# Kernel optimization log

Measured on AMD Instinct MI355X. Metric: run time of the kernel, lower is better.

## Reference

```python
import jax, jax.numpy as jnp
import numpy as np

LAMBDA_D = 250.0
POS_MARGIN = 1.0
NEG_MARGIN = 0.2
BLOCK = 8          # block_size in the original
DIST_THRESH = 7.5  # correspondence threshold in pixels
EPS = 1e-12        # F.normalize eps


def _l2_normalize(x, axis):
    # matches torch.nn.functional.normalize: x / max(||x||_2, eps)
    n = jnp.linalg.norm(x, axis=axis, keepdims=True)
    return x / jnp.maximum(n, EPS)


def setup_inputs() -> dict:
    key = jax.random.key(0)
    k1, k2, k3 = jax.random.split(key, 3)
    b, d, hc, wc = 2, 256, 60, 80  # 480x640 image, block 8
    desc = jax.random.normal(k1, (b, d, hc, wc), dtype=jnp.float32)
    wrap_desc = jax.random.normal(k2, (b, d, hc, wc), dtype=jnp.float32)
    # realistic near-identity homographies (random H would warp everything off-image)
    H = jnp.eye(3, dtype=jnp.float32)[None] + 0.02 * jax.random.normal(k3, (b, 3, 3), dtype=jnp.float32)
    return {"desc": desc, "wrap_desc": wrap_desc, "H": H}


def reference(desc, wrap_desc, H):
    b, d, hc, wc = desc.shape
    n = hc * wc

    # cell-center coordinates in (row, col) order, shape (hc, wc, 2)
    coords = jnp.stack(
        jnp.meshgrid(jnp.arange(hc), jnp.arange(wc), indexing="ij"), axis=-1
    ).astype(jnp.float32) * BLOCK + BLOCK // 2

    # homogeneous (x, y, 1) points, shape (n, 3)
    xy1 = jnp.concatenate(
        [coords[..., 1:2], coords[..., 0:1], jnp.ones((hc, wc, 1), jnp.float32)],
        axis=-1,
    ).reshape(n, 3)

    # warp by homography: (b, n, 3)
    w = jnp.einsum("bij,nj->bni", H, xy1)
    wxy = w[..., :2] / w[..., 2:3]                       # (b, n, 2) in (x, y)
    warp = jnp.stack([wxy[..., 1], wxy[..., 0]], axis=-1).reshape(b, hc, wc, 2)  # (row, col)

    # distance between warped query centers and all cell centers: (b, hc, wc, hc, wc)
    dist = jnp.linalg.norm(coords[None, None, None] - warp[:, :, :, None, None, :], axis=-1)
    S = (dist <= DIST_THRESH).astype(desc.dtype)

    # unit-normalized descriptors, channel-last
    dn = _l2_normalize(jnp.transpose(desc, (0, 2, 3, 1)), axis=-1)       # (b, hc, wc, d)
    wn = _l2_normalize(jnp.transpose(wrap_desc, (0, 2, 3, 1)), axis=-1)  # (b, hc, wc, d)

    # full correlation volume via batched GEMM (same math as broadcast-sum)
    dot = jax.nn.relu(jnp.einsum("bijd,bkld->bijkl", dn, wn))           # (b,hc,wc,hc,wc)

    # normalize over warped-cell axis (k, l), then over query-cell axis (i, j)
    dot = _l2_normalize(dot.reshape(b, hc, wc, n), axis=3).reshape(b, hc, wc, hc, wc)
    dot = _l2_normalize(dot.reshape(b, n, hc, wc), axis=1).reshape(b, hc, wc, hc, wc)

    loss = LAMBDA_D * S * jax.nn.relu(POS_MARGIN - dot) + (1.0 - S) * jax.nn.relu(dot - NEG_MARGIN)
    # sum over (i,j,k,l) per image / n^2, then sum over batch == total sum / n^2
    return jnp.sum(loss) / float(n * n)
```

## Files before the change

### kernel.cpp

```cpp
#include <hip/hip_runtime.h>

#define HC 60
#define WCC 80
#define NCELL 4800
#define NP 4864
#define NB 38
#define DCH 256
#define BATCH 2
#define QT 64

typedef _Float16 half8 __attribute__((ext_vector_type(8)));
typedef float f32x4 __attribute__((ext_vector_type(4)));

__device__ __forceinline__ void gload_lds16(const void* gp, void* lp) {
  __builtin_amdgcn_global_load_lds(
      (const __attribute__((address_space(1))) void*)gp,
      (__attribute__((address_space(3))) void*)lp, 16, 0, 0);
}

__global__ __launch_bounds__(256) void warp_kernel(const float* __restrict__ H,
                                                   float* __restrict__ wout) {
  int idx = blockIdx.x * 256 + threadIdx.x;
  if (idx >= BATCH * NP) return;
  int b = idx / NP;
  int q = idx - b * NP;
  float wr = 1e9f, wc = 1e9f;
  if (q < NCELL) {
    int i = q / WCC;
    int j = q - i * WCC;
    float x = (float)(j * 8 + 4);
    float y = (float)(i * 8 + 4);
    const float* h = H + b * 9;
    float w0 = h[0] * x + h[1] * y + h[2];
    float w1 = h[3] * x + h[4] * y + h[5];
    float w2 = h[6] * x + h[7] * y + h[8];
    wr = w1 / w2;
    wc = w0 / w2;
  }
  wout[2 * idx]     = wr;
  wout[2 * idx + 1] = wc;
}

__global__ __launch_bounds__(256) void normalize_kernel(
    const float* __restrict__ desc, const float* __restrict__ wdesc,
    _Float16* __restrict__ dnp, _Float16* __restrict__ wnp) {
  __shared__ _Float16 vt[DCH][QT + 2];
  __shared__ float pss[4][QT];
  __shared__ float invq[QT];
  const int q0 = blockIdx.x * QT;
  const int which = blockIdx.y;
  const int b = blockIdx.z;
  const float* in = which ? wdesc : desc;
  _Float16* out = which ? wnp : dnp;
  const int tx = threadIdx.x & 63;
  const int ty = threadIdx.x >> 6;
  const int q = q0 + tx;
  float ss = 0.f;
  for (int cc = 0; cc < DCH / 4; ++cc) {
    const int c = cc * 4 + ty;
    float v = (q < NCELL) ? in[((size_t)b * DCH + c) * NCELL + q] : 0.f;
    vt[c][tx] = (_Float16)v;
    ss += v * v;
  }
  pss[ty][tx] = ss;
  __syncthreads();
  if (ty == 0) {
    float tot = pss[0][tx] + pss[1][tx] + pss[2][tx] + pss[3][tx];
    invq[tx] = 1.f / fmaxf(sqrtf(tot), 1e-12f);
  }
  __syncthreads();
  for (int it = 0; it < QT; ++it) {
    out[((size_t)b * NP + q0 + it) * DCH + threadIdx.x] =
        (_Float16)((float)vt[threadIdx.x][it] * invq[it]);
  }
}

union GemmSmem {
  struct { _Float16 As[128][64]; _Float16 Bs[128][64]; } g;
  _Float16 rp[128][132];
};

template <int MODE, bool STOREU>
__global__ __launch_bounds__(256) void gemm_kernel(
    const _Float16* __restrict__ A, const _Float16* __restrict__ Bm,
    const float* __restrict__ invr, const float* __restrict__ colscale,
    const float* __restrict__ warp, float* __restrict__ sqacc,
    float* __restrict__ lossp, _Float16* __restrict__ uout) {
  __shared__ GemmSmem sm;
  const int tid = threadIdx.x;
  const int wave = tid >> 6;
  const int lane = tid & 63;
  const int batch = blockIdx.z;
  const int row0 = blockIdx.y * 128;
  const int col0 = blockIdx.x * 128;
  const _Float16* Ab = A + ((size_t)batch * NP + row0) * DCH;
  const _Float16* Bb = Bm + ((size_t)batch * NP + col0) * DCH;

  const int wq_r = wave >> 1;
  const int wq_c = wave & 1;
  const int g = lane >> 4;
  const int cL = lane & 15;

  f32x4 acc[4][4] = {};

  const int srow = lane >> 3;
  const int scol = lane & 7;
  const int sc_swz = (scol ^ srow) * 8;

  for (int ks = 0; ks < 4; ++ks) {
#pragma unroll
    for (int c = 0; c < 4; ++c) {
      const int chunk = wave * 4 + c;
      const int r = chunk * 8 + srow;
      gload_lds16(Ab + (size_t)r * DCH + ks * 64 + sc_swz,
                  (char*)(&sm.g.As[0][0]) + chunk * 1024);
      gload_lds16(Bb + (size_t)r * DCH + ks * 64 + sc_swz,
                  (char*)(&sm.g.Bs[0][0]) + chunk * 1024);
    }
    __syncthreads();
#pragma unroll
    for (int kk = 0; kk < 2; ++kk) {
      half8 af[4], bf[4];
#pragma unroll
      for (int m = 0; m < 4; ++m) {
        const int row = wq_r * 64 + m * 16 + cL;
        const int c16 = (kk * 4 + g) ^ (row & 7);
        af[m] = *reinterpret_cast<const half8*>(
            (const char*)(&sm.g.As[0][0]) + row * 128 + c16 * 16);
      }
#pragma unroll
      for (int n = 0; n < 4; ++n) {
        const int row = wq_c * 64 + n * 16 + cL;
        const int c16 = (kk * 4 + g) ^ (row & 7);
        bf[n] = *reinterpret_cast<const half8*>(
            (const char*)(&sm.g.Bs[0][0]) + row * 128 + c16 * 16);
      }
#pragma unroll
      for (int m = 0; m < 4; ++m)
#pragma unroll
        for (int n = 0; n < 4; ++n)
          acc[m][n] =
              __builtin_amdgcn_mfma_f32_16x16x32_f16(af[m], bf[n], acc[m][n], 0, 0, 0);
    }
    __syncthreads();
  }

  if (MODE == 0 || MODE == 1) {
    float cs[4];
    if (MODE == 1) {
#pragma unroll
      for (int n = 0; n < 4; ++n)
        cs[n] = colscale[(size_t)batch * NP + col0 + wq_c * 64 + n * 16 + cL];
    }
    float rs[4][4];
#pragma unroll
    for (int m = 0; m < 4; ++m)
#pragma unroll
      for (int j = 0; j < 4; ++j) rs[m][j] = 0.f;
#pragma unroll
    for (int m = 0; m < 4; ++m)
#pragma unroll
      for (int n = 0; n < 4; ++n)
#pragma unroll
        for (int j = 0; j < 4; ++j) {
          float u = fmaxf(acc[m][n][j], 0.f);
          if (MODE == 1) u *= cs[n];
          rs[m][j] += u * u;
        }
#pragma unroll
    for (int m = 0; m < 4; ++m)
#pragma unroll
      for (int j = 0; j < 4; ++j) {
        float v = rs[m][j];
        v += __shfl_xor(v, 1, 64);
        v += __shfl_xor(v, 2, 64);
        v += __shfl_xor(v, 4, 64);
        v += __shfl_xor(v, 8, 64);
        if (cL == 0)
          atomicAdd(&sqacc[(size_t)batch * NP + row0 + wq_r * 64 + m * 16 + g * 4 + j], v);
      }
    if (STOREU) {
#pragma unroll
      for (int m = 0; m < 4; ++m)
#pragma unroll
        for (int n = 0; n < 4; ++n)
#pragma unroll
          for (int j = 0; j < 4; ++j)
            sm.rp[wq_r * 64 + m * 16 + g * 4 + j][wq_c * 64 + n * 16 + cL] =
                (_Float16)fmaxf(acc[m][n][j], 0.f);
      __syncthreads();
      const int rl = tid >> 4;
      const int uu = tid & 15;
#pragma unroll
      for (int p = 0; p < 8; ++p) {
        const int row = p * 16 + rl;
        half8 hv = *reinterpret_cast<const half8*>(&sm.rp[row][uu * 8]);
        *reinterpret_cast<half8*>(
            &uout[((size_t)batch * NP + row0 + row) * NP + col0 + uu * 8]) = hv;
      }
    }
  } else if (MODE == 2) {
    float cy[4], cx[4], ic[4];
    int cvalid[4];
#pragma unroll
    for (int n = 0; n < 4; ++n) {
      int ct = col0 + wq_c * 64 + n * 16 + cL;
      cvalid[n] = (ct < NCELL);
      int tk = ct / WCC;
      int tl = ct - tk * WCC;
      cy[n] = (float)(tk * 8 + 4);
      cx[n] = (float)(tl * 8 + 4);
      ic[n] = colscale[(size_t)batch * NP + ct];
    }
    float lsum = 0.f;
#pragma unroll
    for (int m = 0; m < 4; ++m)
#pragma unroll
      for (int j = 0; j < 4; ++j) {
        const int rq = row0 + wq_r * 64 + m * 16 + g * 4 + j;
        if (rq < NCELL) {
          const float ir = invr[(size_t)batch * NP + rq];
          const float wr = warp[((size_t)batch * NP + rq) * 2];
          const float wcol = warp[((size_t)batch * NP + rq) * 2 + 1];
#pragma unroll
          for (int n = 0; n < 4; ++n) {
            if (cvalid[n]) {
              float u = fmaxf(acc[m][n][j], 0.f);
              float v = u * ir * ic[n];
              float dr = cy[n] - wr;
              float dc = cx[n] - wcol;
              float pos = 250.f * fmaxf(1.f - v, 0.f);
              float neg = fmaxf(v - 0.2f, 0.f);
              lsum += (dr * dr + dc * dc <= 56.25f) ? pos : neg;
            }
          }
        }
      }
#pragma unroll
    for (int s = 1; s < 64; s <<= 1) lsum += __shfl_xor(lsum, s, 64);
    if (lane == 0) {
      int slot = (((batch * NB + blockIdx.y) * NB + blockIdx.x) << 2) | wave;
      lossp[slot] = lsum;
    }
  }
}

__global__ __launch_bounds__(256) void passB_kernel(const _Float16* __restrict__ u,
                                                    const float* __restrict__ r2,
                                                    float* __restrict__ c2) {
  const int b = blockIdx.z;
  const int lt = threadIdx.x & 63;
  const int lq = threadIdx.x >> 6;
  const int t0 = blockIdx.x * 512 + lt * 8;
  const int q0 = blockIdx.y * 64 + lq * 16;
  float s[8];
#pragma unroll
  for (int i = 0; i < 8; ++i) s[i] = 0.f;
  if (t0 < NP) {
    const _Float16* up = u + ((size_t)b * NP + q0) * NP + t0;
    const float* r2p = r2 + b * NP + q0;
#pragma unroll 4
    for (int q = 0; q < 16; ++q) {
      const float ir = 1.f / fmaxf(sqrtf(r2p[q]), 1e-12f);
      half8 h = *reinterpret_cast<const half8*>(up + (size_t)q * NP);
#pragma unroll
      for (int i = 0; i < 8; ++i) {
        float v = (float)h[i] * ir;
        s[i] += v * v;
      }
    }
  }
  __shared__ float red[4][64][9];
#pragma unroll
  for (int i = 0; i < 8; ++i) red[lq][lt][i] = s[i];
  __syncthreads();
  if (lq == 0 && t0 < NP) {
#pragma unroll
    for (int i = 0; i < 8; ++i) {
      float tot = red[0][lt][i] + red[1][lt][i] + red[2][lt][i] + red[3][lt][i];
      atomicAdd(&c2[b * NP + t0 + i], tot);
    }
  }
}

__global__ __launch_bounds__(256) void passC_kernel(const _Float16* __restrict__ u,
                                                    const float* __restrict__ r2,
                                                    const float* __restrict__ c2,
                                                    const float* __restrict__ warp,
                                                    float* __restrict__ lossp) {
  const int b = blockIdx.z;
  const int lt = threadIdx.x & 63;
  const int lq = threadIdx.x >> 6;
  const int t0 = blockIdx.x * 512 + lt * 8;
  const int q0 = blockIdx.y * 128 + lq * 32;
  float cy[8], cx[8], ic[8];
  bool val[8];
  const bool act = (t0 < NP);
#pragma unroll
  for (int i = 0; i < 8; ++i) {
    const int t = act ? (t0 + i) : 0;
    val[i] = act && (t < NCELL);
    const int tk = t / WCC;
    const int tl = t - tk * WCC;
    cy[i] = (float)(tk * 8 + 4);
    cx[i] = (float)(tl * 8 + 4);
    ic[i] = val[i] ? 1.f / fmaxf(sqrtf(c2[b * NP + t]), 1e-12f) : 0.f;
  }
  float lsum = 0.f;
  if (act) {
    const _Float16* up = u + ((size_t)b * NP + q0) * NP + t0;
#pragma unroll 4
    for (int q = 0; q < 32; ++q) {
      const int qq = q0 + q;
      const float ir = 1.f / fmaxf(sqrtf(r2[b * NP + qq]), 1e-12f);
      const float wr = warp[(size_t)(b * NP + qq) * 2];
      const float wc = warp[(size_t)(b * NP + qq) * 2 + 1];
      half8 h = *reinterpret_cast<const half8*>(up + (size_t)q * NP);
#pragma unroll
      for (int i = 0; i < 8; ++i) {
        if (val[i]) {
          float v = (float)h[i] * ir * ic[i];
          float dr = cy[i] - wr;
          float dc = cx[i] - wc;
          float pos = 250.f * fmaxf(1.f - v, 0.f);
          float neg = fmaxf(v - 0.2f, 0.f);
          lsum += (dr * dr + dc * dc <= 56.25f) ? pos : neg;
        }
      }
    }
  }
#pragma unroll
  for (int s = 1; s < 64; s <<= 1) lsum += __shfl_xor(lsum, s, 64);
  if (lt == 0)
    lossp[(((b * NB + blockIdx.y) * 10 + blockIdx.x) << 2) | lq] = lsum;
}

__global__ void finalize_inv(const float* __restrict__ sq, float* __restrict__ inv,
                             int count) {
  int i = blockIdx.x * 256 + threadIdx.x;
  if (i < count) inv[i] = 1.f / fmaxf(sqrtf(sq[i]), 1e-12f);
}

__global__ __launch_bounds__(1024) void loss_reduce(const float* __restrict__ lossp,
                                                    float* __restrict__ out, int count) {
  double s = 0.0;
  for (int i = threadIdx.x; i < count; i += 1024) s += (double)lossp[i];
#pragma unroll
  for (int k = 1; k < 64; k <<= 1) s += __shfl_xor(s, k, 64);
  __shared__ double sd[16];
  if ((threadIdx.x & 63) == 0) sd[threadIdx.x >> 6] = s;
  __syncthreads();
  if (threadIdx.x == 0) {
    double t = 0.0;
    for (int w = 0; w < 16; ++w) t += sd[w];
    out[0] = (float)(t / ((double)NCELL * (double)NCELL));
  }
}

extern "C" void kernel_launch(void* const* d_in, const int* in_sizes, int n_in,
                              void* d_out, int out_size, void* d_ws, size_t ws_size,
                              hipStream_t stream) {
  const float* desc  = (const float*)d_in[0];
  const float* wdesc = (const float*)d_in[1];
  const float* H     = (const float*)d_in[2];
  char* ws = (char*)d_ws;

  constexpr size_t SZ_HALF = (size_t)BATCH * NP * DCH * sizeof(_Float16);
  constexpr size_t SZ_WARP = (size_t)BATCH * NP * 2 * sizeof(float);
  constexpr size_t SZ_VEC  = (size_t)BATCH * NP * sizeof(float);
  constexpr size_t SZ_LOSS = (size_t)BATCH * NB * 10 * 4 * sizeof(float);
  constexpr size_t SZ_U    = (size_t)BATCH * NP * NP * sizeof(_Float16);
  constexpr size_t OFF_DNP  = 0;
  constexpr size_t OFF_WNP  = OFF_DNP + SZ_HALF;
  constexpr size_t OFF_WARP = OFF_WNP + SZ_HALF;
  constexpr size_t OFF_R2   = OFF_WARP + SZ_WARP;
  constexpr size_t OFF_C2   = OFF_R2 + SZ_VEC;
  constexpr size_t OFF_INVR = OFF_C2 + SZ_VEC;
  constexpr size_t OFF_INVC = OFF_INVR + SZ_VEC;
  constexpr size_t OFF_LOSS = OFF_INVC + SZ_VEC;
  constexpr size_t SZ_LOSS2 = (size_t)BATCH * NB * NB * 4 * sizeof(float);
  constexpr size_t OFF_U    = OFF_LOSS + (SZ_LOSS > SZ_LOSS2 ? SZ_LOSS : SZ_LOSS2);
  constexpr size_t TOTAL    = OFF_U + SZ_U;

  _Float16* dnp = (_Float16*)(ws + OFF_DNP);
  _Float16* wnp = (_Float16*)(ws + OFF_WNP);
  float* warp = (float*)(ws + OFF_WARP);
  float* r2   = (float*)(ws + OFF_R2);
  float* c2   = (float*)(ws + OFF_C2);
  float* invr = (float*)(ws + OFF_INVR);
  float* invc = (float*)(ws + OFF_INVC);
  float* lossp = (float*)(ws + OFF_LOSS);
  _Float16* u = (_Float16*)(ws + OFF_U);

  hipMemsetAsync(r2, 0, 2 * SZ_VEC, stream);

  warp_kernel<<<dim3((BATCH * NP + 255) / 256), 256, 0, stream>>>(H, warp);
  normalize_kernel<<<dim3(NP / QT, 2, BATCH), 256, 0, stream>>>(desc, wdesc, dnp, wnp);

  dim3 gg(NB, NB, BATCH);
  if (ws_size >= TOTAL) {
    gemm_kernel<0, true><<<gg, 256, 0, stream>>>(dnp, wnp, nullptr, nullptr, nullptr,
                                                 r2, nullptr, u);
    passB_kernel<<<dim3(10, 76, BATCH), 256, 0, stream>>>(u, r2, c2);
    passC_kernel<<<dim3(10, NB, BATCH), 256, 0, stream>>>(u, r2, c2, warp, lossp);
    loss_reduce<<<1, 1024, 0, stream>>>(lossp, (float*)d_out, BATCH * NB * 10 * 4);
  } else {
    gemm_kernel<0, false><<<gg, 256, 0, stream>>>(dnp, wnp, nullptr, nullptr, nullptr,
                                                  r2, nullptr, nullptr);
    finalize_inv<<<(BATCH * NP + 255) / 256, 256, 0, stream>>>(r2, invr, BATCH * NP);
    gemm_kernel<1, false><<<gg, 256, 0, stream>>>(wnp, dnp, nullptr, invr, nullptr,
                                                  c2, nullptr, nullptr);
    finalize_inv<<<(BATCH * NP + 255) / 256, 256, 0, stream>>>(c2, invc, BATCH * NP);
    gemm_kernel<2, false><<<gg, 256, 0, stream>>>(dnp, wnp, invr, invc, warp,
                                                  nullptr, lossp, nullptr);
    loss_reduce<<<1, 1024, 0, stream>>>(lossp, (float*)d_out, BATCH * NB * NB * 4);
  }
}
```

Baseline: 241.3 us.

## Split normalize into sumsq and transpose kernels, retile passB/passC, inline warp

```diff
diff --git a/kernel.cpp b/kernel.cpp
--- a/kernel.cpp
+++ b/kernel.cpp
@@ -7,10 +7,10 @@
 #define NB 38
 #define DCH 256
 #define BATCH 2
-#define QT 64
 
 typedef _Float16 half8 __attribute__((ext_vector_type(8)));
 typedef float f32x4 __attribute__((ext_vector_type(4)));
+typedef float float4v __attribute__((ext_vector_type(4)));
 
 __device__ __forceinline__ void gload_lds16(const void* gp, void* lp) {
   __builtin_amdgcn_global_load_lds(
@@ -41,37 +41,69 @@
   wout[2 * idx + 1] = wc;
 }
 
-__global__ __launch_bounds__(256) void normalize_kernel(
+__global__ __launch_bounds__(256) void sumsq_kernel(const float* __restrict__ desc,
+                                                    const float* __restrict__ wdesc,
+                                                    float* __restrict__ ss) {
+  const int b = blockIdx.z;
+  const int tensor = blockIdx.y >> 2;
+  const int c0 = (blockIdx.y & 3) * 64;
+  const int q = blockIdx.x * 256 + threadIdx.x;
+  const float* in = tensor ? wdesc : desc;
+  float s = 0.f;
+  if (q < NCELL) {
+    const float* p = in + ((size_t)b * DCH + c0) * NCELL + q;
+#pragma unroll 16
+    for (int c = 0; c < 64; ++c) {
+      float v = p[(size_t)c * NCELL];
+      s += v * v;
+    }
+  }
+  atomicAdd(&ss[((size_t)tensor * BATCH + b) * NP + q], s);
+}
+
+__global__ __launch_bounds__(256) void transpose_kernel(
     const float* __restrict__ desc, const float* __restrict__ wdesc,
-    _Float16* __restrict__ dnp, _Float16* __restrict__ wnp) {
-  __shared__ _Float16 vt[DCH][QT + 2];
-  __shared__ float pss[4][QT];
-  __shared__ float invq[QT];
-  const int q0 = blockIdx.x * QT;
-  const int which = blockIdx.y;
+    const float* __restrict__ ss, _Float16* __restrict__ dnp,
+    _Float16* __restrict__ wnp) {
+  __shared__ _Float16 vt[256][66];
+  __shared__ float iss[256];
   const int b = blockIdx.z;
-  const float* in = which ? wdesc : desc;
-  _Float16* out = which ? wnp : dnp;
-  const int tx = threadIdx.x & 63;
-  const int ty = threadIdx.x >> 6;
-  const int q = q0 + tx;
-  float ss = 0.f;
-  for (int cc = 0; cc < DCH / 4; ++cc) {
-    const int c = cc * 4 + ty;
-    float v = (q < NCELL) ? in[((size_t)b * DCH + c) * NCELL + q] : 0.f;
-    vt[c][tx] = (_Float16)v;
-    ss += v * v;
-  }
-  pss[ty][tx] = ss;
+  const int tensor = blockIdx.y >> 2;
+  const int c0 = (blockIdx.y & 3) * 64;
+  const int q0 = blockIdx.x * 256;
+  const float* in = tensor ? wdesc : desc;
+  _Float16* out = tensor ? wnp : dnp;
+  const int wave = threadIdx.x >> 6;
+  const int lane = threadIdx.x & 63;
+  {
+    float v = ss[((size_t)tensor * BATCH + b) * NP + q0 + threadIdx.x];
+    iss[threadIdx.x] = 1.f / fmaxf(sqrtf(v), 1e-12f);
+  }
+#pragma unroll
+  for (int i = 0; i < 16; ++i) {
+    const int c = c0 + wave * 16 + i;
+    const int q = q0 + lane * 4;
+    float4v v = {0.f, 0.f, 0.f, 0.f};
+    if (q + 3 < NCELL) {
+      v = *reinterpret_cast<const float4v*>(in + ((size_t)b * DCH + c) * NCELL + q);
+    } else {
+#pragma unroll
+      for (int k = 0; k < 4; ++k)
+        if (q + k < NCELL) v[k] = in[((size_t)b * DCH + c) * NCELL + q + k];
+    }
+#pragma unroll
+    for (int k = 0; k < 4; ++k) vt[lane * 4 + k][wave * 16 + i] = (_Float16)v[k];
+  }
   __syncthreads();
-  if (ty == 0) {
-    float tot = pss[0][tx] + pss[1][tx] + pss[2][tx] + pss[3][tx];
-    invq[tx] = 1.f / fmaxf(sqrtf(tot), 1e-12f);
-  }
-  __syncthreads();
-  for (int it = 0; it < QT; ++it) {
-    out[((size_t)b * NP + q0 + it) * DCH + threadIdx.x] =
-        (_Float16)((float)vt[threadIdx.x][it] * invq[it]);
+#pragma unroll
+  for (int p = 0; p < 8; ++p) {
+    const int qr = p * 32 + wave * 8 + (lane >> 3);
+    const int cl = (lane & 7) * 8;
+    const float is = iss[qr];
+    half8 hv;
+#pragma unroll
+    for (int k = 0; k < 8; ++k) hv[k] = (_Float16)((float)vt[qr][cl + k] * is);
+    *reinterpret_cast<half8*>(out + ((size_t)b * NP + q0 + qr) * DCH + c0 + cl) = hv;
   }
 }
 
@@ -252,21 +284,27 @@
   const int lt = threadIdx.x & 63;
   const int lq = threadIdx.x >> 6;
   const int t0 = blockIdx.x * 512 + lt * 8;
-  const int q0 = blockIdx.y * 64 + lq * 16;
+  const int q0 = blockIdx.y * 32 + lq * 8;
+  const bool act = (t0 < NP);
+  half8 h[8];
+  const _Float16* up = u + ((size_t)b * NP + q0) * NP + t0;
+  if (act) {
+#pragma unroll
+    for (int j = 0; j < 8; ++j)
+      h[j] = *reinterpret_cast<const half8*>(up + (size_t)j * NP);
+  }
   float s[8];
 #pragma unroll
   for (int i = 0; i < 8; ++i) s[i] = 0.f;
-  if (t0 < NP) {
-    const _Float16* up = u + ((size_t)b * NP + q0) * NP + t0;
-    const float* r2p = r2 + b * NP + q0;
-#pragma unroll 4
-    for (int q = 0; q < 16; ++q) {
-      const float ir = 1.f / fmaxf(sqrtf(r2p[q]), 1e-12f);
-      half8 h = *reinterpret_cast<const half8*>(up + (size_t)q * NP);
+  if (act) {
+    const float* rp = r2 + b * NP + q0;
+#pragma unroll
+    for (int j = 0; j < 8; ++j) {
+      const float sq = 1.f / fmaxf(rp[j], 1e-24f);
 #pragma unroll
       for (int i = 0; i < 8; ++i) {
-        float v = (float)h[i] * ir;
-        s[i] += v * v;
+        float v = (float)h[j][i];
+        s[i] += v * v * sq;
       }
     }
   }
@@ -274,7 +312,7 @@
 #pragma unroll
   for (int i = 0; i < 8; ++i) red[lq][lt][i] = s[i];
   __syncthreads();
-  if (lq == 0 && t0 < NP) {
+  if (lq == 0 && act) {
 #pragma unroll
     for (int i = 0; i < 8; ++i) {
       float tot = red[0][lt][i] + red[1][lt][i] + red[2][lt][i] + red[3][lt][i];
@@ -286,16 +324,26 @@
 __global__ __launch_bounds__(256) void passC_kernel(const _Float16* __restrict__ u,
                                                     const float* __restrict__ r2,
                                                     const float* __restrict__ c2,
-                                                    const float* __restrict__ warp,
+                                                    const float* __restrict__ H,
                                                     float* __restrict__ lossp) {
   const int b = blockIdx.z;
   const int lt = threadIdx.x & 63;
   const int lq = threadIdx.x >> 6;
   const int t0 = blockIdx.x * 512 + lt * 8;
-  const int q0 = blockIdx.y * 128 + lq * 32;
+  const int q0 = blockIdx.y * 32 + lq * 8;
+  const bool act = (t0 < NP);
+  half8 h[8];
+  const _Float16* up = u + ((size_t)b * NP + q0) * NP + t0;
+  if (act) {
+#pragma unroll
+    for (int j = 0; j < 8; ++j)
+      h[j] = *reinterpret_cast<const half8*>(up + (size_t)j * NP);
+  }
+  float hm[9];
+#pragma unroll
+  for (int k = 0; k < 9; ++k) hm[k] = H[b * 9 + k];
   float cy[8], cx[8], ic[8];
   bool val[8];
-  const bool act = (t0 < NP);
 #pragma unroll
   for (int i = 0; i < 8; ++i) {
     const int t = act ? (t0 + i) : 0;
@@ -308,23 +356,30 @@
   }
   float lsum = 0.f;
   if (act) {
-    const _Float16* up = u + ((size_t)b * NP + q0) * NP + t0;
-#pragma unroll 4
-    for (int q = 0; q < 32; ++q) {
-      const int qq = q0 + q;
-      const float ir = 1.f / fmaxf(sqrtf(r2[b * NP + qq]), 1e-12f);
-      const float wr = warp[(size_t)(b * NP + qq) * 2];
-      const float wc = warp[(size_t)(b * NP + qq) * 2 + 1];
-      half8 h = *reinterpret_cast<const half8*>(up + (size_t)q * NP);
-#pragma unroll
-      for (int i = 0; i < 8; ++i) {
-        if (val[i]) {
-          float v = (float)h[i] * ir * ic[i];
-          float dr = cy[i] - wr;
-          float dc = cx[i] - wc;
-          float pos = 250.f * fmaxf(1.f - v, 0.f);
-          float neg = fmaxf(v - 0.2f, 0.f);
-          lsum += (dr * dr + dc * dc <= 56.25f) ? pos : neg;
+#pragma unroll
+    for (int j = 0; j < 8; ++j) {
+      const int qq = q0 + j;
+      if (qq < NCELL) {
+        const float ir = 1.f / fmaxf(sqrtf(r2[b * NP + qq]), 1e-12f);
+        const int qi = qq / WCC;
+        const int qj = qq - qi * WCC;
+        const float x = (float)(qj * 8 + 4);
+        const float y = (float)(qi * 8 + 4);
+        const float w0 = hm[0] * x + hm[1] * y + hm[2];
+        const float w1 = hm[3] * x + hm[4] * y + hm[5];
+        const float w2 = hm[6] * x + hm[7] * y + hm[8];
+        const float wr = w1 / w2;
+        const float wc = w0 / w2;
+#pragma unroll
+        for (int i = 0; i < 8; ++i) {
+          if (val[i]) {
+            float v = (float)h[j][i] * ir * ic[i];
+            float dr = cy[i] - wr;
+            float dc = cx[i] - wc;
+            float pos = 250.f * fmaxf(1.f - v, 0.f);
+            float neg = fmaxf(v - 0.2f, 0.f);
+            lsum += (dr * dr + dc * dc <= 56.25f) ? pos : neg;
+          }
         }
       }
     }
@@ -332,7 +387,7 @@
 #pragma unroll
   for (int s = 1; s < 64; s <<= 1) lsum += __shfl_xor(lsum, s, 64);
   if (lt == 0)
-    lossp[(((b * NB + blockIdx.y) * 10 + blockIdx.x) << 2) | lq] = lsum;
+    lossp[(((b * 152 + blockIdx.y) * 10 + blockIdx.x) << 2) | lq] = lsum;
 }
 
 __global__ void finalize_inv(const float* __restrict__ sq, float* __restrict__ inv,
@@ -368,23 +423,24 @@
   constexpr size_t SZ_HALF = (size_t)BATCH * NP * DCH * sizeof(_Float16);
   constexpr size_t SZ_WARP = (size_t)BATCH * NP * 2 * sizeof(float);
   constexpr size_t SZ_VEC  = (size_t)BATCH * NP * sizeof(float);
-  constexpr size_t SZ_LOSS = (size_t)BATCH * NB * 10 * 4 * sizeof(float);
+  constexpr size_t SZ_LOSS = 16384 * sizeof(float);
   constexpr size_t SZ_U    = (size_t)BATCH * NP * NP * sizeof(_Float16);
   constexpr size_t OFF_DNP  = 0;
   constexpr size_t OFF_WNP  = OFF_DNP + SZ_HALF;
   constexpr size_t OFF_WARP = OFF_WNP + SZ_HALF;
-  constexpr size_t OFF_R2   = OFF_WARP + SZ_WARP;
+  constexpr size_t OFF_SS   = OFF_WARP + SZ_WARP;
+  constexpr size_t OFF_R2   = OFF_SS + 2 * SZ_VEC;
   constexpr size_t OFF_C2   = OFF_R2 + SZ_VEC;
   constexpr size_t OFF_INVR = OFF_C2 + SZ_VEC;
   constexpr size_t OFF_INVC = OFF_INVR + SZ_VEC;
   constexpr size_t OFF_LOSS = OFF_INVC + SZ_VEC;
-  constexpr size_t SZ_LOSS2 = (size_t)BATCH * NB * NB * 4 * sizeof(float);
-  constexpr size_t OFF_U    = OFF_LOSS + (SZ_LOSS > SZ_LOSS2 ? SZ_LOSS : SZ_LOSS2);
+  constexpr size_t OFF_U    = OFF_LOSS + SZ_LOSS;
   constexpr size_t TOTAL    = OFF_U + SZ_U;
 
   _Float16* dnp = (_Float16*)(ws + OFF_DNP);
   _Float16* wnp = (_Float16*)(ws + OFF_WNP);
   float* warp = (float*)(ws + OFF_WARP);
+  float* ss   = (float*)(ws + OFF_SS);
   float* r2   = (float*)(ws + OFF_R2);
   float* c2   = (float*)(ws + OFF_C2);
   float* invr = (float*)(ws + OFF_INVR);
@@ -392,19 +448,20 @@
   float* lossp = (float*)(ws + OFF_LOSS);
   _Float16* u = (_Float16*)(ws + OFF_U);
 
-  hipMemsetAsync(r2, 0, 2 * SZ_VEC, stream);
-
-  warp_kernel<<<dim3((BATCH * NP + 255) / 256), 256, 0, stream>>>(H, warp);
-  normalize_kernel<<<dim3(NP / QT, 2, BATCH), 256, 0, stream>>>(desc, wdesc, dnp, wnp);
+  hipMemsetAsync(ss, 0, 4 * SZ_VEC, stream);
+
+  sumsq_kernel<<<dim3(19, 8, BATCH), 256, 0, stream>>>(desc, wdesc, ss);
+  transpose_kernel<<<dim3(19, 8, BATCH), 256, 0, stream>>>(desc, wdesc, ss, dnp, wnp);
 
   dim3 gg(NB, NB, BATCH);
   if (ws_size >= TOTAL) {
     gemm_kernel<0, true><<<gg, 256, 0, stream>>>(dnp, wnp, nullptr, nullptr, nullptr,
                                                  r2, nullptr, u);
-    passB_kernel<<<dim3(10, 76, BATCH), 256, 0, stream>>>(u, r2, c2);
-    passC_kernel<<<dim3(10, NB, BATCH), 256, 0, stream>>>(u, r2, c2, warp, lossp);
-    loss_reduce<<<1, 1024, 0, stream>>>(lossp, (float*)d_out, BATCH * NB * 10 * 4);
+    passB_kernel<<<dim3(10, 152, BATCH), 256, 0, stream>>>(u, r2, c2);
+    passC_kernel<<<dim3(10, 152, BATCH), 256, 0, stream>>>(u, r2, c2, H, lossp);
+    loss_reduce<<<1, 1024, 0, stream>>>(lossp, (float*)d_out, BATCH * 152 * 10 * 4);
   } else {
+    warp_kernel<<<dim3((BATCH * NP + 255) / 256), 256, 0, stream>>>(H, warp);
     gemm_kernel<0, false><<<gg, 256, 0, stream>>>(dnp, wnp, nullptr, nullptr, nullptr,
                                                   r2, nullptr, nullptr);
     finalize_inv<<<(BATCH * NP + 255) / 256, 256, 0, stream>>>(r2, invr, BATCH * NP);
```

Result: slower. 265.6 us (+10.1%).
